# Performance work log

Measured on AMD Instinct MI355X. Metric: run time of the kernel, lower is better.

Reference implementation:

```python
import jax, jax.numpy as jnp
import numpy as np

B, D, L, E, H = 8192, 1024, 256, 16, 400

def setup_inputs() -> dict:
    key = jax.random.key(0)
    ks = jax.random.split(key, 6)
    s1 = 1.0 / np.sqrt(D)
    s2 = 1.0 / np.sqrt(H)
    return {
        "x": jax.random.normal(ks[0], (B, D), dtype=jnp.float32),
        "angle_idx": jax.random.randint(ks[1], (B,), 0, E, dtype=jnp.int64),
        "W1": jax.random.uniform(ks[2], (E, D, H), jnp.float32, -s1, s1),
        "b1": jax.random.uniform(ks[3], (E, H), jnp.float32, -s1, s1),
        "W2": jax.random.uniform(ks[4], (E, H, 2 * L), jnp.float32, -s2, s2),
        "b2": jax.random.uniform(ks[5], (E, 2 * L), jnp.float32, -s2, s2),
    }

def reference(x, angle_idx, W1, b1, W2, b2):
    # Dense all-experts compute, then per-sample select (jit-friendly MoE dispatch).
    # h1: [E, B, H]
    h1 = jax.nn.relu(jnp.einsum('bd,edh->ebh', x, W1) + b1[:, None, :])
    # h: [E, B, 2L]
    h = jnp.einsum('ebh,ehk->ebk', h1, W2) + b2[:, None, :]
    sel = h[angle_idx, jnp.arange(x.shape[0])]  # [B, 2L], each row from its routed expert
    half = sel.shape[1] // 2
    z_mu, z_logvar = sel[:, :half], sel[:, half:]
    return (z_mu, z_logvar)
```

## Files before the change

kernel.cpp:

```cpp
#include <hip/hip_runtime.h>
#include <hip/hip_bf16.h>
#include <cstdint>
#include <cstddef>

#define B_N 8192
#define D_K 1024
#define H_N 400
#define HP  416
#define K2_N 512
#define E_N 16
#define L_N 256
#define TM 64
#define PAD_ROWS (B_N + E_N * TM)
#define NTILES (PAD_ROWS / TM)

typedef short bf16x8 __attribute__((ext_vector_type(8)));
typedef float f32x4 __attribute__((ext_vector_type(4)));

#define GLDS(gp, lp) __builtin_amdgcn_global_load_lds( \
    (const __attribute__((address_space(1))) unsigned int*)(gp), \
    (__attribute__((address_space(3))) unsigned int*)(lp), 16, 0, 0)

static __device__ __forceinline__ unsigned short f2bf(float f) {
  union { float f; unsigned int u; } c; c.f = f;
  unsigned int u = c.u + 0x7fffu + ((c.u >> 16) & 1u);
  return (unsigned short)(u >> 16);
}
static __device__ __forceinline__ unsigned int pkbf(float a, float b) {
  union { __hip_bfloat162 v; unsigned int u; } c;
  c.v = __float22bfloat162_rn(make_float2(a, b));
  return c.u;
}

__global__ __launch_bounds__(256) void prep_kernel(const float* __restrict__ W1,
                                                   const float* __restrict__ W2,
                                                   const float* __restrict__ x,
                                                   const int* __restrict__ idx,
                                                   unsigned short* __restrict__ Wt1,
                                                   unsigned short* __restrict__ Wt2,
                                                   unsigned short* __restrict__ xc,
                                                   int* __restrict__ off_al,
                                                   int* __restrict__ cnt_al,
                                                   int* __restrict__ order) {
  const int bid = blockIdx.x;
  const int t = threadIdx.x;
  if (bid < 32) {
    const int hb = bid;
    __shared__ int totW[4][E_N], preW[4][E_N];
    __shared__ int totL[E_N], preL[E_N], offsL[E_N], curL[E_N];
    const int wv = t >> 6;
    if (t < 64) { totW[t >> 4][t & 15] = 0; preW[t >> 4][t & 15] = 0; }
    __syncthreads();
#pragma unroll 1
    for (int c = 0; c < 32; ++c) {
      const int e0 = idx[c * 256 + t];
      atomicAdd(&totW[wv][e0], 1);
      if (c < hb) atomicAdd(&preW[wv][e0], 1);
    }
    __syncthreads();
    if (t < E_N) {
      totL[t] = totW[0][t] + totW[1][t] + totW[2][t] + totW[3][t];
      preL[t] = preW[0][t] + preW[1][t] + preW[2][t] + preW[3][t];
    }
    __syncthreads();
    if (t == 0) {
      int acc = 0;
      for (int e = 0; e < E_N; ++e) {
        offsL[e] = acc;
        if (hb == 0) off_al[e] = acc;
        acc += ((totL[e] + TM - 1) / TM) * TM;
      }
      if (hb == 0) off_al[E_N] = acc;
    }
    __syncthreads();
    if (t < E_N) {
      curL[t] = offsL[t] + preL[t];
      if (hb == 0) cnt_al[t] = totL[t];
    }
    __syncthreads();
    const int b = hb * 256 + t;
    const int e = idx[b];
    const int slot = atomicAdd(&curL[e], 1);
    order[slot] = b;
    if (hb == 0) *(uint2*)(xc + (size_t)B_N * D_K + t * 4) = make_uint2(0, 0);
  } else if (bid < 2720) {
    const int u = bid - 32;
    __shared__ unsigned short Ls[64][72];
    const float* S; unsigned short* Dt; int K, N, Kd, Nd, k0, n0;
    if (u < 1792) {
      int e = u / 112, r = u % 112;
      k0 = (r % 16) * 64; n0 = (r / 16) * 64;
      S = W1 + (size_t)e * D_K * H_N; Dt = Wt1 + (size_t)e * HP * D_K;
      K = D_K; N = H_N; Kd = D_K; Nd = HP;
    } else {
      int t2 = u - 1792; int e = t2 / 56, r = t2 % 56;
      k0 = (r % 7) * 64; n0 = (r / 7) * 64;
      S = W2 + (size_t)e * H_N * K2_N; Dt = Wt2 + (size_t)e * K2_N * HP;
      K = H_N; N = K2_N; Kd = HP; Nd = K2_N;
    }
    const int kk = t >> 4;
    const int nn = (t & 15) * 4;
    float4 v[4];
#pragma unroll
    for (int p = 0; p < 4; ++p) {
      int k = k0 + p * 16 + kk;
      int n = n0 + nn;
      v[p] = make_float4(0.f, 0.f, 0.f, 0.f);
      if (k < K && n + 3 < N) v[p] = *(const float4*)(S + (size_t)k * N + n);
    }
#pragma unroll
    for (int p = 0; p < 4; ++p) {
      Ls[nn + 0][p * 16 + kk] = f2bf(v[p].x);
      Ls[nn + 1][p * 16 + kk] = f2bf(v[p].y);
      Ls[nn + 2][p * 16 + kk] = f2bf(v[p].z);
      Ls[nn + 3][p * 16 + kk] = f2bf(v[p].w);
    }
    __syncthreads();
    const int n2 = t >> 3;
    const int ch = t & 7;
#pragma unroll
    for (int p = 0; p < 2; ++p) {
      int n = n0 + p * 32 + n2;
      int k = k0 + ch * 8;
      if (n < Nd && k < Kd)
        *(uint4*)(Dt + (size_t)n * Kd + k) = *(const uint4*)&Ls[p * 32 + n2][ch * 8];
    }
  } else {
    const int xb = bid - 2720;
    const float* S = x + (size_t)xb * 16 * D_K;
    unsigned short* Dp = xc + (size_t)xb * 16 * D_K;
#pragma unroll
    for (int i = 0; i < 16; ++i) {
      float4 v = *(const float4*)(S + i * D_K + t * 4);
      uint2 o; o.x = pkbf(v.x, v.y); o.y = pkbf(v.z, v.w);
      *(uint2*)(Dp + i * D_K + t * 4) = o;
    }
  }
}

static __device__ __forceinline__ void swz_decode(int bx, int by, int& mt, int& nb) {
  const int L = bx + NTILES * by;
  const int vid = (L & 7) * 72 + (L >> 3);
  mt = vid >> 2;
  nb = vid & 3;
}

__global__ __launch_bounds__(256) void gemm1_kernel(const unsigned short* __restrict__ xc,
                                                    const unsigned short* __restrict__ Wt1,
                                                    const float* __restrict__ b1,
                                                    const int* __restrict__ off_al,
                                                    const int* __restrict__ cnt_al,
                                                    const int* __restrict__ order,
                                                    unsigned short* __restrict__ h1buf) {
  __shared__ unsigned short As[2 * 2 * 2048];
  __shared__ unsigned short Bs[2 * 2 * 4096];
  __shared__ int offs[E_N + 1];
  __shared__ int rowidx[TM];
  const int tid = threadIdx.x;
  int mt, nb;
  swz_decode(blockIdx.x, blockIdx.y, mt, nb);
  const int m0 = mt * TM;
  if (tid <= E_N) offs[tid] = off_al[tid];
  __syncthreads();
  if (m0 >= offs[E_N]) return;
  int e = 0;
  while (m0 >= offs[e + 1]) ++e;
  if (tid < TM) {
    const bool valid = (m0 + tid) < (offs[e] + cnt_al[e]);
    rowidx[tid] = valid ? order[m0 + tid] : B_N;
  }
  __syncthreads();
  const unsigned short* Wt1e = Wt1 + (size_t)e * HP * D_K;

  const int l = tid & 63, w = tid >> 6;
  const int r4 = l >> 2;
  const int sg = (r4 ^ (r4 >> 2)) & 3;
  const int g8 = ((l & 3) ^ sg) * 8;
  const int t0 = nb * 8 + 2 * w;
  const bool act0 = (t0 < 25);
  const bool act1 = (t0 + 1 < 25);
  const unsigned short* gA = xc + (size_t)rowidx[16 * w + r4] * D_K + g8;
  const unsigned short* gB0 = Wt1e + (size_t)(t0 * 16 + r4) * D_K + g8;
  const unsigned short* gB1 = gB0 + (size_t)16 * D_K;

  const int ln = l & 15, q = l >> 4;
  const int sr = (ln ^ (ln >> 2)) & 3;
  const int cq = (q ^ sr) * 8;

  f32x4 acc[4][2] = {};

#pragma unroll
  for (int ks = 0; ks < 2; ++ks) {
    GLDS(gA + ks * 32, &As[ks * 2048 + 16 * w * 32]);
    if (act0) GLDS(gB0 + ks * 32, &Bs[ks * 4096 + (2 * w + 0) * 512]);
    if (act1) GLDS(gB1 + ks * 32, &Bs[ks * 4096 + (2 * w + 1) * 512]);
  }

  for (int k0 = 0; k0 < D_K; k0 += 64) {
    const int cur = (k0 >> 6) & 1;
    const int nxt = cur ^ 1;
    __syncthreads();
    if (k0 + 64 < D_K) {
#pragma unroll
      for (int ks = 0; ks < 2; ++ks) {
        const int kg = k0 + 64 + ks * 32;
        GLDS(gA + kg, &As[nxt * 4096 + ks * 2048 + 16 * w * 32]);
        if (act0) GLDS(gB0 + kg, &Bs[nxt * 8192 + ks * 4096 + (2 * w + 0) * 512]);
        if (act1) GLDS(gB1 + kg, &Bs[nxt * 8192 + ks * 4096 + (2 * w + 1) * 512]);
      }
    }
    if (act0) {
#pragma unroll
      for (int ks = 0; ks < 2; ++ks) {
        const unsigned short* Ab = &As[cur * 4096 + ks * 2048];
        const unsigned short* Bb = &Bs[cur * 8192 + ks * 4096];
        bf16x8 af[4];
#pragma unroll
        for (int i = 0; i < 4; ++i)
          af[i] = *(const bf16x8*)&Ab[(16 * i + ln) * 32 + cq];
        bf16x8 b0f = *(const bf16x8*)&Bb[(2 * w + 0) * 512 + ln * 32 + cq];
#pragma unroll
        for (int i = 0; i < 4; ++i)
          acc[i][0] = __builtin_amdgcn_mfma_f32_16x16x32_bf16(b0f, af[i], acc[i][0], 0, 0, 0);
        if (act1) {
          bf16x8 b1f = *(const bf16x8*)&Bb[(2 * w + 1) * 512 + ln * 32 + cq];
#pragma unroll
          for (int i = 0; i < 4; ++i)
            acc[i][1] = __builtin_amdgcn_mfma_f32_16x16x32_bf16(b1f, af[i], acc[i][1], 0, 0, 0);
        }
      }
    }
  }

#pragma unroll
  for (int j = 0; j < 2; ++j) {
    if (j == 0 ? act0 : act1) {
      const int n4 = (t0 + j) * 16 + 4 * q;
      const float4 bv = *(const float4*)&b1[e * H_N + n4];
#pragma unroll
      for (int i = 0; i < 4; ++i) {
        const size_t m = (size_t)(m0 + 16 * i + ln);
        uint2 o;
        o.x = pkbf(fmaxf(acc[i][j][0] + bv.x, 0.f), fmaxf(acc[i][j][1] + bv.y, 0.f));
        o.y = pkbf(fmaxf(acc[i][j][2] + bv.z, 0.f), fmaxf(acc[i][j][3] + bv.w, 0.f));
        *(uint2*)&h1buf[m * HP + n4] = o;
      }
    }
  }
}

__global__ __launch_bounds__(256) void gemm2_kernel(const unsigned short* __restrict__ h1buf,
                                                    const unsigned short* __restrict__ Wt2,
                                                    const float* __restrict__ b2,
                                                    const int* __restrict__ off_al,
                                                    const int* __restrict__ cnt_al,
                                                    const int* __restrict__ order,
                                                    float* __restrict__ out) {
  __shared__ unsigned short As[2 * 2 * 2048];
  __shared__ unsigned short Bs[2 * 2 * 4096];
  __shared__ int offs[E_N + 1];
  __shared__ int rowidx[TM];
  const int tid = threadIdx.x;
  int mt, nb;
  swz_decode(blockIdx.x, blockIdx.y, mt, nb);
  const int m0 = mt * TM;
  if (tid <= E_N) offs[tid] = off_al[tid];
  __syncthreads();
  if (m0 >= offs[E_N]) return;
  int e = 0;
  while (m0 >= offs[e + 1]) ++e;
  if (tid < TM) {
    const bool valid = (m0 + tid) < (offs[e] + cnt_al[e]);
    rowidx[tid] = valid ? order[m0 + tid] : -1;
  }
  __syncthreads();
  const unsigned short* Wt2e = Wt2 + (size_t)e * K2_N * HP;

  const int l = tid & 63, w = tid >> 6;
  const int r4 = l >> 2;
  const int sg = (r4 ^ (r4 >> 2)) & 3;
  const int g8 = ((l & 3) ^ sg) * 8;
  const int t0 = nb * 8 + 2 * w;
  const unsigned short* gA = h1buf + (size_t)(m0 + 16 * w + r4) * HP + g8;
  const unsigned short* gB0 = Wt2e + (size_t)(t0 * 16 + r4) * HP + g8;
  const unsigned short* gB1 = gB0 + (size_t)16 * HP;

  const int ln = l & 15, q = l >> 4;
  const int sr = (ln ^ (ln >> 2)) & 3;
  const int cq = (q ^ sr) * 8;

  f32x4 acc[4][2] = {};

#pragma unroll
  for (int ks = 0; ks < 2; ++ks) {
    GLDS(gA + ks * 32, &As[ks * 2048 + 16 * w * 32]);
    GLDS(gB0 + ks * 32, &Bs[ks * 4096 + (2 * w + 0) * 512]);
    GLDS(gB1 + ks * 32, &Bs[ks * 4096 + (2 * w + 1) * 512]);
  }

  for (int k0 = 0; k0 < HP; k0 += 64) {
    const int cur = (k0 >> 6) & 1;
    const int nxt = cur ^ 1;
    __syncthreads();
#pragma unroll
    for (int ks = 0; ks < 2; ++ks) {
      const int kg = k0 + 64 + ks * 32;
      if (kg < HP) {
        GLDS(gA + kg, &As[nxt * 4096 + ks * 2048 + 16 * w * 32]);
        GLDS(gB0 + kg, &Bs[nxt * 8192 + ks * 4096 + (2 * w + 0) * 512]);
        GLDS(gB1 + kg, &Bs[nxt * 8192 + ks * 4096 + (2 * w + 1) * 512]);
      }
    }
#pragma unroll
    for (int ks = 0; ks < 2; ++ks) {
      if (k0 + ks * 32 < HP) {
        const unsigned short* Ab = &As[cur * 4096 + ks * 2048];
        const unsigned short* Bb = &Bs[cur * 8192 + ks * 4096];
        bf16x8 af[4];
#pragma unroll
        for (int i = 0; i < 4; ++i)
          af[i] = *(const bf16x8*)&Ab[(16 * i + ln) * 32 + cq];
        bf16x8 b0f = *(const bf16x8*)&Bb[(2 * w + 0) * 512 + ln * 32 + cq];
#pragma unroll
        for (int i = 0; i < 4; ++i)
          acc[i][0] = __builtin_amdgcn_mfma_f32_16x16x32_bf16(b0f, af[i], acc[i][0], 0, 0, 0);
        bf16x8 b1f = *(const bf16x8*)&Bb[(2 * w + 1) * 512 + ln * 32 + cq];
#pragma unroll
        for (int i = 0; i < 4; ++i)
          acc[i][1] = __builtin_amdgcn_mfma_f32_16x16x32_bf16(b1f, af[i], acc[i][1], 0, 0, 0);
      }
    }
  }

#pragma unroll
  for (int j = 0; j < 2; ++j) {
    const int n4 = (t0 + j) * 16 + 4 * q;
    const float4 bv = *(const float4*)&b2[e * K2_N + n4];
#pragma unroll
    for (int i = 0; i < 4; ++i) {
      const int s = rowidx[16 * i + ln];
      if (s >= 0) {
        float4 v;
        v.x = acc[i][j][0] + bv.x;
        v.y = acc[i][j][1] + bv.y;
        v.z = acc[i][j][2] + bv.z;
        v.w = acc[i][j][3] + bv.w;
        if (n4 < L_N) *(float4*)&out[(size_t)s * L_N + n4] = v;
        else          *(float4*)&out[(size_t)(B_N + s) * L_N + (n4 - L_N)] = v;
      }
    }
  }
}

extern "C" void kernel_launch(void* const* d_in, const int* in_sizes, int n_in,
                              void* d_out, int out_size, void* d_ws, size_t ws_size,
                              hipStream_t stream) {
  const float* x   = (const float*)d_in[0];
  const int*   idx = (const int*)d_in[1];
  const float* W1  = (const float*)d_in[2];
  const float* b1  = (const float*)d_in[3];
  const float* W2  = (const float*)d_in[4];
  const float* b2  = (const float*)d_in[5];
  float* out = (float*)d_out;

  char* ws = (char*)d_ws;
  int* off_al = (int*)(ws + 0);
  int* cnt_al = (int*)(ws + 128);
  int* order  = (int*)(ws + 2240);
  unsigned short* xc  = (unsigned short*)(ws + 39104);
  unsigned short* h1  = (unsigned short*)(ws + 16818368);
  unsigned short* Wt1 = (unsigned short*)(ws + 24486080);
  unsigned short* Wt2 = (unsigned short*)(ws + 38117568);

  prep_kernel<<<3232, 256, 0, stream>>>(W1, W2, x, idx, Wt1, Wt2, xc,
                                        off_al, cnt_al, order);
  gemm1_kernel<<<dim3(NTILES, 4), 256, 0, stream>>>(xc, Wt1, b1, off_al, cnt_al, order, h1);
  gemm2_kernel<<<dim3(NTILES, 4), 256, 0, stream>>>(h1, Wt2, b2, off_al, cnt_al, order, out);
}
```

Measured before the change: 158.6 us.

## Fuse fp32-to-bf16 conversion of x into gemm1 A-tile loading

Drops the separate x-to-bf16 conversion pass from the prep kernel. gemm1 now reads fp32 rows of x directly into registers, converts them to bf16 and writes them into LDS, with a register-prefetch pipeline that replaces the global_load_lds path for A. This removes the 16 MB xc write and read round trip and 512 prep blocks. In exchange, each x row is read in fp32 four times, once per N-block, and the A path goes through registers and VALU conversion instead of direct LDS loads.

Measured after the change: 203.5 us. 28.3% more time.

```diff
diff --git a/kernel.cpp b/kernel.cpp
--- a/kernel.cpp
+++ b/kernel.cpp
@@ -34,11 +34,9 @@
 
 __global__ __launch_bounds__(256) void prep_kernel(const float* __restrict__ W1,
                                                    const float* __restrict__ W2,
-                                                   const float* __restrict__ x,
                                                    const int* __restrict__ idx,
                                                    unsigned short* __restrict__ Wt1,
                                                    unsigned short* __restrict__ Wt2,
-                                                   unsigned short* __restrict__ xc,
                                                    int* __restrict__ off_al,
                                                    int* __restrict__ cnt_al,
                                                    int* __restrict__ order) {
@@ -82,8 +80,7 @@
     const int e = idx[b];
     const int slot = atomicAdd(&curL[e], 1);
     order[slot] = b;
-    if (hb == 0) *(uint2*)(xc + (size_t)B_N * D_K + t * 4) = make_uint2(0, 0);
-  } else if (bid < 2720) {
+  } else {
     const int u = bid - 32;
     __shared__ unsigned short Ls[64][72];
     const float* S; unsigned short* Dt; int K, N, Kd, Nd, k0, n0;
@@ -125,16 +122,6 @@
       if (n < Nd && k < Kd)
         *(uint4*)(Dt + (size_t)n * Kd + k) = *(const uint4*)&Ls[p * 32 + n2][ch * 8];
     }
-  } else {
-    const int xb = bid - 2720;
-    const float* S = x + (size_t)xb * 16 * D_K;
-    unsigned short* Dp = xc + (size_t)xb * 16 * D_K;
-#pragma unroll
-    for (int i = 0; i < 16; ++i) {
-      float4 v = *(const float4*)(S + i * D_K + t * 4);
-      uint2 o; o.x = pkbf(v.x, v.y); o.y = pkbf(v.z, v.w);
-      *(uint2*)(Dp + i * D_K + t * 4) = o;
-    }
   }
 }
 
@@ -145,7 +132,7 @@
   nb = vid & 3;
 }
 
-__global__ __launch_bounds__(256) void gemm1_kernel(const unsigned short* __restrict__ xc,
+__global__ __launch_bounds__(256) void gemm1_kernel(const float* __restrict__ x,
                                                     const unsigned short* __restrict__ Wt1,
                                                     const float* __restrict__ b1,
                                                     const int* __restrict__ off_al,
@@ -167,7 +154,7 @@
   while (m0 >= offs[e + 1]) ++e;
   if (tid < TM) {
     const bool valid = (m0 + tid) < (offs[e] + cnt_al[e]);
-    rowidx[tid] = valid ? order[m0 + tid] : B_N;
+    rowidx[tid] = valid ? order[m0 + tid] : -1;
   }
   __syncthreads();
   const unsigned short* Wt1e = Wt1 + (size_t)e * HP * D_K;
@@ -175,12 +162,14 @@
   const int l = tid & 63, w = tid >> 6;
   const int r4 = l >> 2;
   const int sg = (r4 ^ (r4 >> 2)) & 3;
-  const int g8 = ((l & 3) ^ sg) * 8;
+  const int c8 = ((l & 3) ^ sg) * 8;
   const int t0 = nb * 8 + 2 * w;
   const bool act0 = (t0 < 25);
   const bool act1 = (t0 + 1 < 25);
-  const unsigned short* gA = xc + (size_t)rowidx[16 * w + r4] * D_K + g8;
-  const unsigned short* gB0 = Wt1e + (size_t)(t0 * 16 + r4) * D_K + g8;
+  const int ar = rowidx[16 * w + r4];
+  const bool av = (ar >= 0);
+  const float* gAx = x + (size_t)(av ? ar : 0) * D_K + c8;
+  const unsigned short* gB0 = Wt1e + (size_t)(t0 * 16 + r4) * D_K + c8;
   const unsigned short* gB1 = gB0 + (size_t)16 * D_K;
 
   const int ln = l & 15, q = l >> 4;
@@ -188,32 +177,43 @@
   const int cq = (q ^ sr) * 8;
 
   f32x4 acc[4][2] = {};
-
-#pragma unroll
-  for (int ks = 0; ks < 2; ++ks) {
-    GLDS(gA + ks * 32, &As[ks * 2048 + 16 * w * 32]);
-    if (act0) GLDS(gB0 + ks * 32, &Bs[ks * 4096 + (2 * w + 0) * 512]);
-    if (act1) GLDS(gB1 + ks * 32, &Bs[ks * 4096 + (2 * w + 1) * 512]);
-  }
-
-  for (int k0 = 0; k0 < D_K; k0 += 64) {
-    const int cur = (k0 >> 6) & 1;
-    const int nxt = cur ^ 1;
-    __syncthreads();
-    if (k0 + 64 < D_K) {
+  const float4 fz = make_float4(0.f, 0.f, 0.f, 0.f);
+  const int awoff = 16 * w * 32 + r4 * 32 + (l & 3) * 8;
+
+  float4 Alo0[2], Ahi0[2], Alo1[2], Ahi1[2];
+#define ALOAD(P, CH)                                                      \
+  do { _Pragma("unroll")                                                  \
+    for (int ks = 0; ks < 2; ++ks) {                                      \
+      const float* s_ = gAx + (CH) * 64 + ks * 32;                        \
+      Alo##P[ks] = av ? *(const float4*)s_ : fz;                          \
+      Ahi##P[ks] = av ? *(const float4*)(s_ + 4) : fz;                    \
+    } } while (0)
+#define AWRITE(P, BUF)                                                    \
+  do { _Pragma("unroll")                                                  \
+    for (int ks = 0; ks < 2; ++ks) {                                      \
+      uint4 o_;                                                           \
+      o_.x = pkbf(Alo##P[ks].x, Alo##P[ks].y);                            \
+      o_.y = pkbf(Alo##P[ks].z, Alo##P[ks].w);                            \
+      o_.z = pkbf(Ahi##P[ks].x, Ahi##P[ks].y);                            \
+      o_.w = pkbf(Ahi##P[ks].z, Ahi##P[ks].w);                            \
+      *(uint4*)&As[(BUF) * 4096 + ks * 2048 + awoff] = o_;                \
+    } } while (0)
+
+  auto stageB = [&](int chunk, int buf) {
+#pragma unroll
+    for (int ks = 0; ks < 2; ++ks) {
+      const int kg = chunk * 64 + ks * 32;
+      if (act0) GLDS(gB0 + kg, &Bs[buf * 8192 + ks * 4096 + (2 * w + 0) * 512]);
+      if (act1) GLDS(gB1 + kg, &Bs[buf * 8192 + ks * 4096 + (2 * w + 1) * 512]);
+    }
+  };
+
+  auto mfma = [&](int buf) {
+    if (act0) {
 #pragma unroll
       for (int ks = 0; ks < 2; ++ks) {
-        const int kg = k0 + 64 + ks * 32;
-        GLDS(gA + kg, &As[nxt * 4096 + ks * 2048 + 16 * w * 32]);
-        if (act0) GLDS(gB0 + kg, &Bs[nxt * 8192 + ks * 4096 + (2 * w + 0) * 512]);
-        if (act1) GLDS(gB1 + kg, &Bs[nxt * 8192 + ks * 4096 + (2 * w + 1) * 512]);
-      }
-    }
-    if (act0) {
-#pragma unroll
-      for (int ks = 0; ks < 2; ++ks) {
-        const unsigned short* Ab = &As[cur * 4096 + ks * 2048];
-        const unsigned short* Bb = &Bs[cur * 8192 + ks * 4096];
+        const unsigned short* Ab = &As[buf * 4096 + ks * 2048];
+        const unsigned short* Bb = &Bs[buf * 8192 + ks * 4096];
         bf16x8 af[4];
 #pragma unroll
         for (int i = 0; i < 4; ++i)
@@ -230,7 +230,26 @@
         }
       }
     }
-  }
+  };
+
+  ALOAD(0, 0);
+  AWRITE(0, 0);
+  stageB(0, 0);
+  ALOAD(1, 1);
+
+#pragma unroll 1
+  for (int kk = 0; kk < 16; kk += 2) {
+    __syncthreads();
+    if (kk + 2 < 16) ALOAD(0, kk + 2);
+    if (kk + 1 < 16) { AWRITE(1, 1); stageB(kk + 1, 1); }
+    mfma(0);
+    __syncthreads();
+    if (kk + 3 < 16) ALOAD(1, kk + 3);
+    if (kk + 2 < 16) { AWRITE(0, 0); stageB(kk + 2, 0); }
+    mfma(1);
+  }
+#undef ALOAD
+#undef AWRITE
 
 #pragma unroll
   for (int j = 0; j < 2; ++j) {
@@ -367,13 +386,12 @@
   int* off_al = (int*)(ws + 0);
   int* cnt_al = (int*)(ws + 128);
   int* order  = (int*)(ws + 2240);
-  unsigned short* xc  = (unsigned short*)(ws + 39104);
   unsigned short* h1  = (unsigned short*)(ws + 16818368);
   unsigned short* Wt1 = (unsigned short*)(ws + 24486080);
   unsigned short* Wt2 = (unsigned short*)(ws + 38117568);
 
-  prep_kernel<<<3232, 256, 0, stream>>>(W1, W2, x, idx, Wt1, Wt2, xc,
+  prep_kernel<<<2720, 256, 0, stream>>>(W1, W2, idx, Wt1, Wt2,
                                         off_al, cnt_al, order);
-  gemm1_kernel<<<dim3(NTILES, 4), 256, 0, stream>>>(xc, Wt1, b1, off_al, cnt_al, order, h1);
+  gemm1_kernel<<<dim3(NTILES, 4), 256, 0, stream>>>(x, Wt1, b1, off_al, cnt_al, order, h1);
   gemm2_kernel<<<dim3(NTILES, 4), 256, 0, stream>>>(h1, Wt2, b2, off_al, cnt_al, order, out);
 }
```
